# Performance work log

Hardware: AMD Instinct MI355X
Metric: run time of the kernel (lower is better)

Reference implementation:

```python
import jax, jax.numpy as jnp
import numpy as np
from jax import lax

B, C, H, W = 16, 256, 56, 56
GROUPS = 4
K = 3
DILATIONS = (1, 3, 5)
EPS = 1e-5


@jax.custom_vjp
def bin_act(x):
    return jnp.sign(x)

def _bin_act_fwd(x):
    return jnp.sign(x), x

def _bin_act_bwd(x, g):
    grad = jnp.where((x >= -1.0) & (x <= 0.0), 2.0 + 2.0 * x, 0.0) \
         + jnp.where((x > 0.0) & (x <= 1.0), 2.0 - 2.0 * x, 0.0)
    return (grad * g,)

bin_act.defvjp(_bin_act_fwd, _bin_act_bwd)


def _bin_weight(wi):
    # per-output-channel scaling from raw |w|, centered sign, clip-STE
    scale = lax.stop_gradient(jnp.mean(jnp.abs(wi), axis=(1, 2, 3), keepdims=True))
    wc = wi - jnp.mean(wi, axis=(1, 2, 3), keepdims=True)
    clipped = jnp.clip(wc, -1.0, 1.0)
    return lax.stop_gradient(scale * jnp.sign(wc) - clipped) + clipped


def setup_inputs() -> dict:
    key = jax.random.key(0)
    ks = jax.random.split(key, 3)
    x = jax.random.normal(ks[0], (B, C, H, W), dtype=jnp.float32)
    # 3 branches of grouped conv weights: (3, C_out, C_in/groups, K, K)
    w = jax.random.normal(ks[1], (3, C, C // GROUPS, K, K), dtype=jnp.float32) * 0.05
    cb = jax.random.normal(ks[2], (3, C), dtype=jnp.float32) * 0.01
    return {
        "x": x,
        "bias": jnp.zeros((1, C, 1, 1), jnp.float32),   # LearnableBias
        "w": w,
        "cb": cb,                                        # conv biases
        "move1": jnp.zeros((3, C), jnp.float32),
        "alpha": jnp.full((3, C), 0.25, jnp.float32),    # PReLU slopes
        "move2": jnp.zeros((3, C), jnp.float32),
        "gamma": jnp.ones((C,), jnp.float32),            # LayerNorm weight
        "beta": jnp.zeros((C,), jnp.float32),            # LayerNorm bias
    }


def reference(x, bias, w, cb, move1, alpha, move2, gamma, beta):
    xb = x + bias
    xq = bin_act(xb)  # binarized activations, shared across branches
    out = jnp.zeros_like(x)
    for i, d in enumerate(DILATIONS):
        wq = _bin_weight(w[i])
        y = lax.conv_general_dilated(
            xq, wq,
            window_strides=(1, 1),
            padding=[(d, d), (d, d)],  # 'same' for k=3 with dilation d
            rhs_dilation=(d, d),
            dimension_numbers=("NCHW", "OIHW", "NCHW"),
            feature_group_count=GROUPS,
        )
        y = y + cb[i][None, :, None, None]
        # RPReLU: shift, channel-wise PReLU, shift
        y = y - move1[i][None, :, None, None]
        y = jnp.where(y >= 0, y, alpha[i][None, :, None, None] * y)
        y = y + move2[i][None, :, None, None]
        out = out + y
    # LayerNorm over channel dim (equivalent to NHWC last-dim LN)
    mean = jnp.mean(out, axis=1, keepdims=True)
    var = jnp.var(out, axis=1, keepdims=True)
    out = (out - mean) * lax.rsqrt(var + EPS)
    out = out * gamma[None, :, None, None] + beta[None, :, None, None]
    return out
```

## Files before the change

### kernel.cpp

```cpp
#include <hip/hip_runtime.h>
#include <hip/hip_fp16.h>
#include <stdint.h>

static constexpr int Bc = 16, Cc = 256, Hc = 56, Wc = 56, Gc = 4, CGc = 64;
static constexpr int HWc = Hc * Wc;
static constexpr float EPSc = 1e-5f;
static constexpr int ROWP = 72;
static constexpr int COL0 = 8;


static constexpr int SBS = 260;

__global__ __launch_bounds__(256) void k_prep(
    const float* __restrict__ w, const float* __restrict__ x,
    const float* __restrict__ bias, uint64_t* __restrict__ wbits,
    float* __restrict__ scales, uint64_t* __restrict__ abits,
    uint32_t* __restrict__ zero_area) {
  const int t = threadIdx.x;
  if (blockIdx.x < 192) {
    const int io = blockIdx.x * 4 + (t >> 6);
    const int i = io >> 8, o = io & 255;
    const int lane = t & 63;
    const float* wp = w + (size_t)io * 576 + lane * 9;
    float v[9];
    float ssum = 0.f, sabs = 0.f;
#pragma unroll
    for (int k = 0; k < 9; ++k) {
      v[k] = wp[k];
      ssum += v[k];
      sabs += fabsf(v[k]);
    }
#pragma unroll
    for (int off = 32; off > 0; off >>= 1) {
      ssum += __shfl_down(ssum, off);
      sabs += __shfl_down(sabs, off);
    }
    const float mean = __shfl(ssum, 0) * (1.f / 576.f);
    const float scale = __shfl(sabs, 0) * (1.f / 576.f);
#pragma unroll
    for (int k = 0; k < 9; ++k) {
      unsigned long long m = __ballot(v[k] > mean);
      if (lane == 0) wbits[(i * 9 + k) * Cc + o] = m;
    }
    if (lane == 0) scales[io] = scale;
  } else if (blockIdx.x == 192) {
    zero_area[t] = 0;
  } else {
    __shared__ uint8_t sb[Wc * SBS];
    const int bid = blockIdx.x - 193;
    const int b = bid / Hc, h = bid % Hc;
    const float* xb = x + ((size_t)b * Cc) * HWc + h * Wc;
#pragma unroll
    for (int k = 0; k < 14; ++k) {
      const int idx = k * 256 + t;
      const int c = idx / 14, q = idx - c * 14;
      const float4 v = *(const float4*)(xb + (size_t)c * HWc + q * 4);
      const float bc = bias[c];
      sb[(q * 4 + 0) * SBS + c] = (v.x + bc > 0.f);
      sb[(q * 4 + 1) * SBS + c] = (v.y + bc > 0.f);
      sb[(q * 4 + 2) * SBS + c] = (v.z + bc > 0.f);
      sb[(q * 4 + 3) * SBS + c] = (v.w + bc > 0.f);
    }
    __syncthreads();
    for (int idx = t; idx < Gc * ROWP; idx += 256) {
      const int g = idx / ROWP, k = idx - g * ROWP;
      uint64_t word = 0;
      if (k >= COL0 && k < COL0 + Wc) {
        const int ww = k - COL0;
        const uint32_t* p = (const uint32_t*)(sb + ww * SBS + g * 64);
        uint64_t acc = 0;
#pragma unroll
        for (int dw = 0; dw < 16; ++dw) {
          const uint32_t d = p[dw];
          const uint32_t nib = (d | (d >> 7) | (d >> 14) | (d >> 21)) & 0xF;
          acc |= (uint64_t)nib << (4 * dw);
        }
        word = acc;
      }
      abits[(((size_t)b * Gc + g) * Hc + h) * ROWP + k] = word;
    }
  }
}

template <int D>
struct Branch {
  uint64_t wgt[9];
  const uint64_t *r0, *r1, *r2;
  int BM, ZL, ZR;
  float sc, cbm1, al;

  __device__ __forceinline__ void init(const uint64_t* __restrict__ wb,
                                       const uint64_t* rowbase,
                                       const uint64_t* zrowp, int h,
                                       float sc_, float cbm1_, float al_) {
    sc = sc_; cbm1 = cbm1_; al = al_;
    int z[9];
#pragma unroll
    for (int k = 0; k < 9; ++k) {
      wgt[k] = wb[k * Cc];
      z[k] = 64 - 2 * (int)__builtin_popcountll(wgt[k]);
    }
    const bool v0 = (h - D >= 0), v2 = (h + D < Hc);
    r0 = v0 ? (rowbase + (size_t)(h - D) * ROWP) : zrowp;
    r1 = rowbase + (size_t)h * ROWP;
    r2 = v2 ? (rowbase + (size_t)(h + D) * ROWP) : zrowp;
    const int Zrow = (v0 ? 0 : (z[0] + z[1] + z[2])) +
                     (v2 ? 0 : (z[6] + z[7] + z[8]));
    BM = 576 - Zrow;
    ZL = (v0 ? z[0] : 0) + z[3] + (v2 ? z[6] : 0);
    ZR = (v0 ? z[2] : 0) + z[5] + (v2 ? z[8] : 0);
  }

  __device__ __forceinline__ void accum8(int w0, int acc[8]) const {
#pragma unroll
    for (int kh = 0; kh < 3; ++kh) {
      const uint64_t* rp = (kh == 0) ? r0 : (kh == 1 ? r1 : r2);
      uint64_t seg[8 + 2 * D];
#pragma unroll
      for (int j = 0; j < 8 + 2 * D; ++j) seg[j] = rp[w0 - D + j];
#pragma unroll
      for (int ww = 0; ww < 8; ++ww) {
#pragma unroll
        for (int kw = 0; kw < 3; ++kw)
          acc[ww] +=
              (int)__builtin_popcountll(wgt[kh * 3 + kw] ^ seg[ww + D * kw]);
      }
    }
  }

  __device__ __forceinline__ void epi8(int w0, const int acc[8],
                                       float outf[8]) const {
#pragma unroll
    for (int ww = 0; ww < 8; ++ww) {
      const int w = w0 + ww;
      const int B = BM - ((w < D) ? ZL : 0) - ((w >= Wc - D) ? ZR : 0);
      const float y0 = fmaf(sc, (float)(B - 2 * acc[ww]), cbm1);
      outf[ww] += fmaxf(y0, 0.f) + al * fminf(y0, 0.f);
    }
  }
};

static constexpr int TS2 = 58;

__global__ __launch_bounds__(256, 4) void k_conv_ln(
    const uint64_t* __restrict__ abits, const uint64_t* __restrict__ zrowp,
    const uint64_t* __restrict__ wbits, const float* __restrict__ scales,
    const float* __restrict__ cb, const float* __restrict__ mv1,
    const float* __restrict__ al, const float* __restrict__ mv2,
    const float* __restrict__ gamma, const float* __restrict__ beta,
    float* __restrict__ out) {
  __shared__ __half out_tile[Cc * TS2];
  __shared__ float redu[4][Wc], redq[4][Wc];
  __shared__ float mstat[Wc], rstat[Wc];

  const int bid = blockIdx.x;
  const int b = bid / Hc, h = bid % Hc;
  const int t = threadIdx.x;
  const int gu = __builtin_amdgcn_readfirstlane(t >> 6);

  const uint64_t* rowbase = abits + ((size_t)b * Gc + gu) * Hc * ROWP + COL0;

  Branch<1> b0; Branch<3> b1; Branch<5> b2;
  b0.init(wbits + 0 * 9 * Cc + t, rowbase, zrowp, h, scales[0 * Cc + t],
          cb[0 * Cc + t] - mv1[0 * Cc + t], al[0 * Cc + t]);
  b1.init(wbits + 1 * 9 * Cc + t, rowbase, zrowp, h, scales[1 * Cc + t],
          cb[1 * Cc + t] - mv1[1 * Cc + t], al[1 * Cc + t]);
  b2.init(wbits + 2 * 9 * Cc + t, rowbase, zrowp, h, scales[2 * Cc + t],
          cb[2 * Cc + t] - mv1[2 * Cc + t], al[2 * Cc + t]);
  const float m2sum = mv2[0 * Cc + t] + mv2[1 * Cc + t] + mv2[2 * Cc + t];

  for (int ch = 0; ch < 7; ++ch) {
    const int w0 = ch * 8;
    float outf[8];
#pragma unroll
    for (int ww = 0; ww < 8; ++ww) outf[ww] = m2sum;
    { int acc[8] = {}; b0.accum8(w0, acc); b0.epi8(w0, acc, outf); }
    { int acc[8] = {}; b1.accum8(w0, acc); b1.epi8(w0, acc, outf); }
    { int acc[8] = {}; b2.accum8(w0, acc); b2.epi8(w0, acc, outf); }
#pragma unroll
    for (int ww = 0; ww < 8; ww += 2) {
      __half2 hv;
      hv.x = __float2half(outf[ww]);
      hv.y = __float2half(outf[ww + 1]);
      *(__half2*)&out_tile[t * TS2 + w0 + ww] = hv;
    }
  }
  __syncthreads();

  if (t < 4 * Wc) {
    const int ww = t % Wc;
    const int cq = t / Wc;
    float s = 0.f, sq = 0.f;
#pragma unroll 4
    for (int c = cq * 64; c < cq * 64 + 64; ++c) {
      const float v = __half2float(out_tile[c * TS2 + ww]);
      s += v;
      sq = fmaf(v, v, sq);
    }
    redu[cq][ww] = s;
    redq[cq][ww] = sq;
  }
  __syncthreads();
  if (t < Wc) {
    const float s = redu[0][t] + redu[1][t] + redu[2][t] + redu[3][t];
    const float sq = redq[0][t] + redq[1][t] + redq[2][t] + redq[3][t];
    const float mean = s * (1.f / 256.f);
    const float var = sq * (1.f / 256.f) - mean * mean;
    mstat[t] = mean;
    rstat[t] = rsqrtf(var + EPSc);
  }
  __syncthreads();

  float* base = out + ((size_t)b * Cc * Hc + h) * Wc;
  for (int idx = t; idx < Cc * Wc; idx += 256) {
    const int c = idx / Wc;
    const int ww = idx - c * Wc;
    const float v = __half2float(out_tile[c * TS2 + ww]);
    base[(size_t)c * HWc + ww] = (v - mstat[ww]) * rstat[ww] * gamma[c] + beta[c];
  }
}

extern "C" void kernel_launch(void* const* d_in, const int* in_sizes, int n_in,
                              void* d_out, int out_size, void* d_ws, size_t ws_size,
                              hipStream_t stream) {
  const float* x     = (const float*)d_in[0];
  const float* bias  = (const float*)d_in[1];
  const float* w     = (const float*)d_in[2];
  const float* cb    = (const float*)d_in[3];
  const float* mv1   = (const float*)d_in[4];
  const float* al    = (const float*)d_in[5];
  const float* mv2   = (const float*)d_in[6];
  const float* gamma = (const float*)d_in[7];
  const float* beta  = (const float*)d_in[8];
  float* out = (float*)d_out;

  uint8_t* ws = (uint8_t*)d_ws;
  uint32_t* zero_area = (uint32_t*)ws;
  const uint64_t* zrowp = (const uint64_t*)ws + COL0;
  uint64_t* abits = (uint64_t*)(ws + 1024);
  const size_t abits_bytes = (size_t)Bc * Gc * Hc * ROWP * 8;
  uint64_t* wbits = (uint64_t*)(ws + 1024 + abits_bytes);
  float* scales = (float*)(ws + 1024 + abits_bytes + 6912 * 8);

  hipLaunchKernelGGL(k_prep, dim3(192 + 1 + Bc * Hc), dim3(256), 0, stream,
                     w, x, bias, wbits, scales, abits, zero_area);
  hipLaunchKernelGGL(k_conv_ln, dim3(Bc * Hc), dim3(256), 0, stream,
                     abits, zrowp, wbits, scales, cb, mv1, al, mv2, gamma, beta,
                     out);
}
```

Measured before the change: 187.7 us.

## Pack activation bits with wave ballots and split conv rows into half-width blocks

The activation packing in the prep kernel now has each lane own one channel and uses wave ballots to build the 64-bit masks directly, replacing the shared-memory byte transpose. It also writes the zero padding columns itself. The conv+LayerNorm kernel now splits each output row into two 28-column halves, which doubles the grid to add parallelism and shrink the shared tile. The cost is that weight bits and per-branch setup are recomputed in both halves, and the chunk size drops to 7 columns with a non-unrolled loop.

Result: slower. 193.4 us (+3.1%).

```diff
diff --git a/kernel.cpp b/kernel.cpp
--- a/kernel.cpp
+++ b/kernel.cpp
@@ -2,14 +2,12 @@
 #include <hip/hip_fp16.h>
 #include <stdint.h>
 
-static constexpr int Bc = 16, Cc = 256, Hc = 56, Wc = 56, Gc = 4, CGc = 64;
+static constexpr int Bc = 16, Cc = 256, Hc = 56, Wc = 56, Gc = 4;
 static constexpr int HWc = Hc * Wc;
 static constexpr float EPSc = 1e-5f;
 static constexpr int ROWP = 72;
 static constexpr int COL0 = 8;
 
-
-static constexpr int SBS = 260;
 
 __global__ __launch_bounds__(256) void k_prep(
     const float* __restrict__ w, const float* __restrict__ x,
@@ -46,38 +44,30 @@
   } else if (blockIdx.x == 192) {
     zero_area[t] = 0;
   } else {
-    __shared__ uint8_t sb[Wc * SBS];
     const int bid = blockIdx.x - 193;
     const int b = bid / Hc, h = bid % Hc;
-    const float* xb = x + ((size_t)b * Cc) * HWc + h * Wc;
+    const int g = t >> 6, lane = t & 63;
+    const float* xp = x + ((size_t)(b * Cc + g * 64 + lane)) * HWc + h * Wc;
+    const float bc = bias[g * 64 + lane];
+    uint64_t* rowp = abits + (((size_t)b * Gc + g) * Hc + h) * ROWP;
+    if (lane < COL0) {
+      rowp[lane] = 0;
+      rowp[COL0 + Wc + lane] = 0;
+    }
 #pragma unroll
     for (int k = 0; k < 14; ++k) {
-      const int idx = k * 256 + t;
-      const int c = idx / 14, q = idx - c * 14;
-      const float4 v = *(const float4*)(xb + (size_t)c * HWc + q * 4);
-      const float bc = bias[c];
-      sb[(q * 4 + 0) * SBS + c] = (v.x + bc > 0.f);
-      sb[(q * 4 + 1) * SBS + c] = (v.y + bc > 0.f);
-      sb[(q * 4 + 2) * SBS + c] = (v.z + bc > 0.f);
-      sb[(q * 4 + 3) * SBS + c] = (v.w + bc > 0.f);
-    }
-    __syncthreads();
-    for (int idx = t; idx < Gc * ROWP; idx += 256) {
-      const int g = idx / ROWP, k = idx - g * ROWP;
-      uint64_t word = 0;
-      if (k >= COL0 && k < COL0 + Wc) {
-        const int ww = k - COL0;
-        const uint32_t* p = (const uint32_t*)(sb + ww * SBS + g * 64);
-        uint64_t acc = 0;
-#pragma unroll
-        for (int dw = 0; dw < 16; ++dw) {
-          const uint32_t d = p[dw];
-          const uint32_t nib = (d | (d >> 7) | (d >> 14) | (d >> 21)) & 0xF;
-          acc |= (uint64_t)nib << (4 * dw);
-        }
-        word = acc;
+      const float4 v = *(const float4*)(xp + k * 4);
+      const unsigned long long m0 = __ballot(v.x + bc > 0.f);
+      const unsigned long long m1 = __ballot(v.y + bc > 0.f);
+      const unsigned long long m2 = __ballot(v.z + bc > 0.f);
+      const unsigned long long m3 = __ballot(v.w + bc > 0.f);
+      if (lane == 0) {
+        ulonglong2 s01, s23;
+        s01.x = m0; s01.y = m1;
+        s23.x = m2; s23.y = m3;
+        *(ulonglong2*)(rowp + COL0 + 4 * k) = s01;
+        *(ulonglong2*)(rowp + COL0 + 4 * k + 2) = s23;
       }
-      abits[(((size_t)b * Gc + g) * Hc + h) * ROWP + k] = word;
     }
   }
 }
@@ -111,15 +101,16 @@
     ZR = (v0 ? z[2] : 0) + z[5] + (v2 ? z[8] : 0);
   }
 
-  __device__ __forceinline__ void accum8(int w0, int acc[8]) const {
+  template <int N>
+  __device__ __forceinline__ void accum(int w0, int acc[N]) const {
 #pragma unroll
     for (int kh = 0; kh < 3; ++kh) {
       const uint64_t* rp = (kh == 0) ? r0 : (kh == 1 ? r1 : r2);
-      uint64_t seg[8 + 2 * D];
-#pragma unroll
-      for (int j = 0; j < 8 + 2 * D; ++j) seg[j] = rp[w0 - D + j];
-#pragma unroll
-      for (int ww = 0; ww < 8; ++ww) {
+      uint64_t seg[N + 2 * D];
+#pragma unroll
+      for (int j = 0; j < N + 2 * D; ++j) seg[j] = rp[w0 - D + j];
+#pragma unroll
+      for (int ww = 0; ww < N; ++ww) {
 #pragma unroll
         for (int kw = 0; kw < 3; ++kw)
           acc[ww] +=
@@ -128,10 +119,11 @@
     }
   }
 
-  __device__ __forceinline__ void epi8(int w0, const int acc[8],
-                                       float outf[8]) const {
-#pragma unroll
-    for (int ww = 0; ww < 8; ++ww) {
+  template <int N>
+  __device__ __forceinline__ void epi(int w0, const int acc[N],
+                                      float outf[N]) const {
+#pragma unroll
+    for (int ww = 0; ww < N; ++ww) {
       const int w = w0 + ww;
       const int B = BM - ((w < D) ? ZL : 0) - ((w >= Wc - D) ? ZR : 0);
       const float y0 = fmaf(sc, (float)(B - 2 * acc[ww]), cbm1);
@@ -140,7 +132,9 @@
   }
 };
 
-static constexpr int TS2 = 58;
+static constexpr int WH = 28;
+static constexpr int TSH = 30;
+static constexpr int NCH = 7;
 
 __global__ __launch_bounds__(256, 4) void k_conv_ln(
     const uint64_t* __restrict__ abits, const uint64_t* __restrict__ zrowp,
@@ -149,12 +143,14 @@
     const float* __restrict__ al, const float* __restrict__ mv2,
     const float* __restrict__ gamma, const float* __restrict__ beta,
     float* __restrict__ out) {
-  __shared__ __half out_tile[Cc * TS2];
-  __shared__ float redu[4][Wc], redq[4][Wc];
-  __shared__ float mstat[Wc], rstat[Wc];
-
-  const int bid = blockIdx.x;
-  const int b = bid / Hc, h = bid % Hc;
+  __shared__ __half out_tile[Cc * TSH];
+  __shared__ float redu[4][WH], redq[4][WH];
+  __shared__ float mstat[WH], rstat[WH];
+
+  const int wh = blockIdx.x & 1;
+  const int bh = blockIdx.x >> 1;
+  const int b = bh / Hc, h = bh % Hc;
+  const int W0 = wh * WH;
   const int t = threadIdx.x;
   const int gu = __builtin_amdgcn_readfirstlane(t >> 6);
 
@@ -169,31 +165,28 @@
           cb[2 * Cc + t] - mv1[2 * Cc + t], al[2 * Cc + t]);
   const float m2sum = mv2[0 * Cc + t] + mv2[1 * Cc + t] + mv2[2 * Cc + t];
 
-  for (int ch = 0; ch < 7; ++ch) {
-    const int w0 = ch * 8;
-    float outf[8];
-#pragma unroll
-    for (int ww = 0; ww < 8; ++ww) outf[ww] = m2sum;
-    { int acc[8] = {}; b0.accum8(w0, acc); b0.epi8(w0, acc, outf); }
-    { int acc[8] = {}; b1.accum8(w0, acc); b1.epi8(w0, acc, outf); }
-    { int acc[8] = {}; b2.accum8(w0, acc); b2.epi8(w0, acc, outf); }
-#pragma unroll
-    for (int ww = 0; ww < 8; ww += 2) {
-      __half2 hv;
-      hv.x = __float2half(outf[ww]);
-      hv.y = __float2half(outf[ww + 1]);
-      *(__half2*)&out_tile[t * TS2 + w0 + ww] = hv;
-    }
+#pragma unroll 1
+  for (int ch = 0; ch < 4; ++ch) {
+    const int w0 = W0 + ch * NCH;
+    float outf[NCH];
+#pragma unroll
+    for (int ww = 0; ww < NCH; ++ww) outf[ww] = m2sum;
+    { int acc[NCH] = {}; b0.accum<NCH>(w0, acc); b0.epi<NCH>(w0, acc, outf); }
+    { int acc[NCH] = {}; b1.accum<NCH>(w0, acc); b1.epi<NCH>(w0, acc, outf); }
+    { int acc[NCH] = {}; b2.accum<NCH>(w0, acc); b2.epi<NCH>(w0, acc, outf); }
+#pragma unroll
+    for (int ww = 0; ww < NCH; ++ww)
+      out_tile[t * TSH + ch * NCH + ww] = __float2half(outf[ww]);
   }
   __syncthreads();
 
-  if (t < 4 * Wc) {
-    const int ww = t % Wc;
-    const int cq = t / Wc;
+  if (t < 4 * WH) {
+    const int ww = t % WH;
+    const int cq = t / WH;
     float s = 0.f, sq = 0.f;
 #pragma unroll 4
     for (int c = cq * 64; c < cq * 64 + 64; ++c) {
-      const float v = __half2float(out_tile[c * TS2 + ww]);
+      const float v = __half2float(out_tile[c * TSH + ww]);
       s += v;
       sq = fmaf(v, v, sq);
     }
@@ -201,7 +194,7 @@
     redq[cq][ww] = sq;
   }
   __syncthreads();
-  if (t < Wc) {
+  if (t < WH) {
     const float s = redu[0][t] + redu[1][t] + redu[2][t] + redu[3][t];
     const float sq = redq[0][t] + redq[1][t] + redq[2][t] + redq[3][t];
     const float mean = s * (1.f / 256.f);
@@ -211,11 +204,11 @@
   }
   __syncthreads();
 
-  float* base = out + ((size_t)b * Cc * Hc + h) * Wc;
-  for (int idx = t; idx < Cc * Wc; idx += 256) {
-    const int c = idx / Wc;
-    const int ww = idx - c * Wc;
-    const float v = __half2float(out_tile[c * TS2 + ww]);
+  float* base = out + ((size_t)b * Cc * Hc + h) * Wc + W0;
+  for (int idx = t; idx < Cc * WH; idx += 256) {
+    const int c = idx / WH;
+    const int ww = idx - c * WH;
+    const float v = __half2float(out_tile[c * TSH + ww]);
     base[(size_t)c * HWc + ww] = (v - mstat[ww]) * rstat[ww] * gamma[c] + beta[c];
   }
 }
@@ -244,7 +237,7 @@
 
   hipLaunchKernelGGL(k_prep, dim3(192 + 1 + Bc * Hc), dim3(256), 0, stream,
                      w, x, bias, wbits, scales, abits, zero_area);
-  hipLaunchKernelGGL(k_conv_ln, dim3(Bc * Hc), dim3(256), 0, stream,
+  hipLaunchKernelGGL(k_conv_ln, dim3(Bc * Hc * 2), dim3(256), 0, stream,
                      abits, zrowp, wbits, scales, cb, mv1, al, mv2, gamma, beta,
                      out);
 }
```

## Replace bit-packed popcount conv with int8 ±1 MFMA matrix products

Applied to the files above, without the earlier changes.

Weights and activations are stored as ±1 int8 bytes instead of packed 64-bit sign words. The grouped dilated conv becomes a sum of 32x32x32 int8 MFMA instructions per tap. The result is the dot product directly, so the zero-padding correction terms go away, and the prep kernel is split into half-channel blocks. This moves the work from VALU popcount onto the matrix cores, at the cost of 8x larger activation storage and more global traffic per row.

Result: slower. 417.3 us (+122.3%).

```diff
diff --git a/kernel.cpp b/kernel.cpp
--- a/kernel.cpp
+++ b/kernel.cpp
@@ -2,19 +2,24 @@
 #include <hip/hip_fp16.h>
 #include <stdint.h>
 
-static constexpr int Bc = 16, Cc = 256, Hc = 56, Wc = 56, Gc = 4, CGc = 64;
+static constexpr int Bc = 16, Cc = 256, Hc = 56, Wc = 56, Gc = 4;
 static constexpr int HWc = Hc * Wc;
 static constexpr float EPSc = 1e-5f;
-static constexpr int ROWP = 72;
+static constexpr int ROWB = 72;
 static constexpr int COL0 = 8;
-
-
-static constexpr int SBS = 260;
+static constexpr int ROWBYTES = ROWB * 64;
+static constexpr int ZBYTES = 8192;
+
+typedef int i32x4 __attribute__((ext_vector_type(4)));
+typedef int i32x16 __attribute__((ext_vector_type(16)));
+
+
+static constexpr int SBS2 = 132;
 
 __global__ __launch_bounds__(256) void k_prep(
     const float* __restrict__ w, const float* __restrict__ x,
-    const float* __restrict__ bias, uint64_t* __restrict__ wbits,
-    float* __restrict__ scales, uint64_t* __restrict__ abits,
+    const float* __restrict__ bias, uint8_t* __restrict__ wbytes,
+    float* __restrict__ scales, uint8_t* __restrict__ abytes,
     uint32_t* __restrict__ zero_area) {
   const int t = threadIdx.x;
   if (blockIdx.x < 192) {
@@ -37,119 +42,91 @@
     }
     const float mean = __shfl(ssum, 0) * (1.f / 576.f);
     const float scale = __shfl(sabs, 0) * (1.f / 576.f);
-#pragma unroll
-    for (int k = 0; k < 9; ++k) {
-      unsigned long long m = __ballot(v[k] > mean);
-      if (lane == 0) wbits[(i * 9 + k) * Cc + o] = m;
-    }
+    const int g = o >> 6, ol = o & 63;
+    uint8_t* dst = wbytes + ((size_t)(i * 4 + g) * 9) * 4096 + ol * 64 + lane;
+#pragma unroll
+    for (int k = 0; k < 9; ++k)
+      dst[k * 4096] = (v[k] > mean) ? (uint8_t)1 : (uint8_t)0xFF;
     if (lane == 0) scales[io] = scale;
   } else if (blockIdx.x == 192) {
-    zero_area[t] = 0;
+    uint4 z;
+    z.x = z.y = z.z = z.w = 0u;
+    ((uint4*)zero_area)[t] = z;
+    ((uint4*)zero_area)[t + 256] = z;
   } else {
-    __shared__ uint8_t sb[Wc * SBS];
+    __shared__ uint8_t sb[Wc * SBS2];
     const int bid = blockIdx.x - 193;
-    const int b = bid / Hc, h = bid % Hc;
-    const float* xb = x + ((size_t)b * Cc) * HWc + h * Wc;
-#pragma unroll
-    for (int k = 0; k < 14; ++k) {
+    const int b = bid / 112;
+    const int rem = bid - b * 112;
+    const int h = rem >> 1, chh = rem & 1;
+    const float* xb = x + ((size_t)(b * Cc + chh * 128)) * HWc + h * Wc;
+#pragma unroll
+    for (int k = 0; k < 7; ++k) {
       const int idx = k * 256 + t;
-      const int c = idx / 14, q = idx - c * 14;
-      const float4 v = *(const float4*)(xb + (size_t)c * HWc + q * 4);
-      const float bc = bias[c];
-      sb[(q * 4 + 0) * SBS + c] = (v.x + bc > 0.f);
-      sb[(q * 4 + 1) * SBS + c] = (v.y + bc > 0.f);
-      sb[(q * 4 + 2) * SBS + c] = (v.z + bc > 0.f);
-      sb[(q * 4 + 3) * SBS + c] = (v.w + bc > 0.f);
+      const int cl = idx / 14, q = idx - cl * 14;
+      const float4 v = *(const float4*)(xb + (size_t)cl * HWc + q * 4);
+      const float bc = bias[chh * 128 + cl];
+      sb[(q * 4 + 0) * SBS2 + cl] = (v.x + bc > 0.f) ? 1 : 0xFF;
+      sb[(q * 4 + 1) * SBS2 + cl] = (v.y + bc > 0.f) ? 1 : 0xFF;
+      sb[(q * 4 + 2) * SBS2 + cl] = (v.z + bc > 0.f) ? 1 : 0xFF;
+      sb[(q * 4 + 3) * SBS2 + cl] = (v.w + bc > 0.f) ? 1 : 0xFF;
     }
     __syncthreads();
-    for (int idx = t; idx < Gc * ROWP; idx += 256) {
-      const int g = idx / ROWP, k = idx - g * ROWP;
-      uint64_t word = 0;
-      if (k >= COL0 && k < COL0 + Wc) {
-        const int ww = k - COL0;
-        const uint32_t* p = (const uint32_t*)(sb + ww * SBS + g * 64);
-        uint64_t acc = 0;
-#pragma unroll
-        for (int dw = 0; dw < 16; ++dw) {
-          const uint32_t d = p[dw];
-          const uint32_t nib = (d | (d >> 7) | (d >> 14) | (d >> 21)) & 0xF;
-          acc |= (uint64_t)nib << (4 * dw);
-        }
-        word = acc;
-      }
-      abits[(((size_t)b * Gc + g) * Hc + h) * ROWP + k] = word;
+    for (int idx = t; idx < 2 * ROWB * 16; idx += 256) {
+      const int gl = idx / (ROWB * 16);
+      const int r = idx - gl * (ROWB * 16);
+      const int wp_ = r >> 4, d4 = r & 15;
+      uint32_t word = 0;
+      if (wp_ >= COL0 && wp_ < COL0 + Wc)
+        word = *(const uint32_t*)(sb + (wp_ - COL0) * SBS2 + gl * 64 + d4 * 4);
+      const int g = chh * 2 + gl;
+      *(uint32_t*)(abytes + ((size_t)((b * Gc + g) * Hc + h)) * ROWBYTES +
+                   wp_ * 64 + d4 * 4) = word;
     }
   }
 }
 
 template <int D>
-struct Branch {
-  uint64_t wgt[9];
-  const uint64_t *r0, *r1, *r2;
-  int BM, ZL, ZR;
-  float sc, cbm1, al;
-
-  __device__ __forceinline__ void init(const uint64_t* __restrict__ wb,
-                                       const uint64_t* rowbase,
-                                       const uint64_t* zrowp, int h,
-                                       float sc_, float cbm1_, float al_) {
-    sc = sc_; cbm1 = cbm1_; al = al_;
-    int z[9];
-#pragma unroll
-    for (int k = 0; k < 9; ++k) {
-      wgt[k] = wb[k * Cc];
-      z[k] = 64 - 2 * (int)__builtin_popcountll(wgt[k]);
-    }
-    const bool v0 = (h - D >= 0), v2 = (h + D < Hc);
-    r0 = v0 ? (rowbase + (size_t)(h - D) * ROWP) : zrowp;
-    r1 = rowbase + (size_t)h * ROWP;
-    r2 = v2 ? (rowbase + (size_t)(h + D) * ROWP) : zrowp;
-    const int Zrow = (v0 ? 0 : (z[0] + z[1] + z[2])) +
-                     (v2 ? 0 : (z[6] + z[7] + z[8]));
-    BM = 576 - Zrow;
-    ZL = (v0 ? z[0] : 0) + z[3] + (v2 ? z[6] : 0);
-    ZR = (v0 ? z[2] : 0) + z[5] + (v2 ? z[8] : 0);
-  }
-
-  __device__ __forceinline__ void accum8(int w0, int acc[8]) const {
-#pragma unroll
-    for (int kh = 0; kh < 3; ++kh) {
-      const uint64_t* rp = (kh == 0) ? r0 : (kh == 1 ? r1 : r2);
-      uint64_t seg[8 + 2 * D];
-#pragma unroll
-      for (int j = 0; j < 8 + 2 * D; ++j) seg[j] = rp[w0 - D + j];
-#pragma unroll
-      for (int ww = 0; ww < 8; ++ww) {
-#pragma unroll
-        for (int kw = 0; kw < 3; ++kw)
-          acc[ww] +=
-              (int)__builtin_popcountll(wgt[kh * 3 + kw] ^ seg[ww + D * kw]);
-      }
-    }
-  }
-
-  __device__ __forceinline__ void epi8(int w0, const int acc[8],
-                                       float outf[8]) const {
-#pragma unroll
-    for (int ww = 0; ww < 8; ++ww) {
-      const int w = w0 + ww;
-      const int B = BM - ((w < D) ? ZL : 0) - ((w >= Wc - D) ? ZR : 0);
-      const float y0 = fmaf(sc, (float)(B - 2 * acc[ww]), cbm1);
-      outf[ww] += fmaxf(y0, 0.f) + al * fminf(y0, 0.f);
-    }
-  }
-};
-
-static constexpr int TS2 = 58;
+__device__ __forceinline__ void branch_accum(
+    const uint8_t* __restrict__ r0, const uint8_t* __restrict__ r1,
+    const uint8_t* __restrict__ r2, const uint8_t* __restrict__ wb,
+    int ot2048, int laneoff, float sc, float cbm1, float alp,
+    float outf0[16], float outf1[16]) {
+  i32x16 ac0 = {0, 0, 0, 0, 0, 0, 0, 0, 0, 0, 0, 0, 0, 0, 0, 0};
+  i32x16 ac1 = {0, 0, 0, 0, 0, 0, 0, 0, 0, 0, 0, 0, 0, 0, 0, 0};
+#pragma unroll
+  for (int tap = 0; tap < 9; ++tap) {
+    const uint8_t* r = (tap < 3) ? r0 : ((tap < 6) ? r1 : r2);
+    const int wsh = (COL0 + D * ((tap % 3) - 1)) * 64 + laneoff;
+#pragma unroll
+    for (int ks = 0; ks < 2; ++ks) {
+      const i32x4 Bf =
+          *(const i32x4*)(wb + tap * 4096 + ot2048 + ks * 32 + laneoff);
+      const i32x4 A0 = *(const i32x4*)(r + wsh + ks * 32);
+      const i32x4 A1 = *(const i32x4*)(r + wsh + 2048 + ks * 32);
+      ac0 = __builtin_amdgcn_mfma_i32_32x32x32_i8(A0, Bf, ac0, 0, 0, 0);
+      ac1 = __builtin_amdgcn_mfma_i32_32x32x32_i8(A1, Bf, ac1, 0, 0, 0);
+    }
+  }
+#pragma unroll
+  for (int q = 0; q < 16; ++q) {
+    const float y0 = fmaf(sc, (float)ac0[q], cbm1);
+    outf0[q] += fmaxf(y0, 0.f) + alp * fminf(y0, 0.f);
+    const float y1 = fmaf(sc, (float)ac1[q], cbm1);
+    outf1[q] += fmaxf(y1, 0.f) + alp * fminf(y1, 0.f);
+  }
+}
+
+static constexpr int TS = 60;
 
 __global__ __launch_bounds__(256, 4) void k_conv_ln(
-    const uint64_t* __restrict__ abits, const uint64_t* __restrict__ zrowp,
-    const uint64_t* __restrict__ wbits, const float* __restrict__ scales,
+    const uint8_t* __restrict__ abytes, const uint8_t* __restrict__ zb,
+    const uint8_t* __restrict__ wbytes, const float* __restrict__ scales,
     const float* __restrict__ cb, const float* __restrict__ mv1,
     const float* __restrict__ al, const float* __restrict__ mv2,
     const float* __restrict__ gamma, const float* __restrict__ beta,
     float* __restrict__ out) {
-  __shared__ __half out_tile[Cc * TS2];
+  __shared__ __half out_tile[Cc * TS];
   __shared__ float redu[4][Wc], redq[4][Wc];
   __shared__ float mstat[Wc], rstat[Wc];
 
@@ -157,32 +134,47 @@
   const int b = bid / Hc, h = bid % Hc;
   const int t = threadIdx.x;
   const int gu = __builtin_amdgcn_readfirstlane(t >> 6);
-
-  const uint64_t* rowbase = abits + ((size_t)b * Gc + gu) * Hc * ROWP + COL0;
-
-  Branch<1> b0; Branch<3> b1; Branch<5> b2;
-  b0.init(wbits + 0 * 9 * Cc + t, rowbase, zrowp, h, scales[0 * Cc + t],
-          cb[0 * Cc + t] - mv1[0 * Cc + t], al[0 * Cc + t]);
-  b1.init(wbits + 1 * 9 * Cc + t, rowbase, zrowp, h, scales[1 * Cc + t],
-          cb[1 * Cc + t] - mv1[1 * Cc + t], al[1 * Cc + t]);
-  b2.init(wbits + 2 * 9 * Cc + t, rowbase, zrowp, h, scales[2 * Cc + t],
-          cb[2 * Cc + t] - mv1[2 * Cc + t], al[2 * Cc + t]);
-  const float m2sum = mv2[0 * Cc + t] + mv2[1 * Cc + t] + mv2[2 * Cc + t];
-
-  for (int ch = 0; ch < 7; ++ch) {
-    const int w0 = ch * 8;
-    float outf[8];
-#pragma unroll
-    for (int ww = 0; ww < 8; ++ww) outf[ww] = m2sum;
-    { int acc[8] = {}; b0.accum8(w0, acc); b0.epi8(w0, acc, outf); }
-    { int acc[8] = {}; b1.accum8(w0, acc); b1.epi8(w0, acc, outf); }
-    { int acc[8] = {}; b2.accum8(w0, acc); b2.epi8(w0, acc, outf); }
-#pragma unroll
-    for (int ww = 0; ww < 8; ww += 2) {
-      __half2 hv;
-      hv.x = __float2half(outf[ww]);
-      hv.y = __float2half(outf[ww + 1]);
-      *(__half2*)&out_tile[t * TS2 + w0 + ww] = hv;
+  const int lane = t & 63, lane31 = lane & 31;
+  const int laneoff = lane31 * 64 + (lane >> 5) * 16;
+
+  const uint8_t* ab_g = abytes + (size_t)((b * Gc + gu) * Hc) * ROWBYTES;
+  const uint8_t* r1m = (h - 1 >= 0) ? ab_g + (size_t)(h - 1) * ROWBYTES : zb;
+  const uint8_t* rmd = ab_g + (size_t)h * ROWBYTES;
+  const uint8_t* r1p = (h + 1 < Hc) ? ab_g + (size_t)(h + 1) * ROWBYTES : zb;
+  const uint8_t* r3m = (h - 3 >= 0) ? ab_g + (size_t)(h - 3) * ROWBYTES : zb;
+  const uint8_t* r3p = (h + 3 < Hc) ? ab_g + (size_t)(h + 3) * ROWBYTES : zb;
+  const uint8_t* r5m = (h - 5 >= 0) ? ab_g + (size_t)(h - 5) * ROWBYTES : zb;
+  const uint8_t* r5p = (h + 5 < Hc) ? ab_g + (size_t)(h + 5) * ROWBYTES : zb;
+
+  const uint8_t* wb0 = wbytes + (size_t)(0 * Gc + gu) * 9 * 4096;
+  const uint8_t* wb1 = wbytes + (size_t)(1 * Gc + gu) * 9 * 4096;
+  const uint8_t* wb2 = wbytes + (size_t)(2 * Gc + gu) * 9 * 4096;
+
+#pragma unroll 1
+  for (int ot = 0; ot < 2; ++ot) {
+    const int o = gu * 64 + ot * 32 + lane31;
+    const float sc0 = scales[o], sc1 = scales[256 + o], sc2 = scales[512 + o];
+    const float c0 = cb[o] - mv1[o];
+    const float c1 = cb[256 + o] - mv1[256 + o];
+    const float c2 = cb[512 + o] - mv1[512 + o];
+    const float a0 = al[o], a1 = al[256 + o], a2 = al[512 + o];
+    const float m2s = mv2[o] + mv2[256 + o] + mv2[512 + o];
+    float outf0[16], outf1[16];
+#pragma unroll
+    for (int q = 0; q < 16; ++q) {
+      outf0[q] = m2s;
+      outf1[q] = m2s;
+    }
+    const int ot2048 = ot * 2048;
+    branch_accum<1>(r1m, rmd, r1p, wb0, ot2048, laneoff, sc0, c0, a0, outf0, outf1);
+    branch_accum<3>(r3m, rmd, r3p, wb1, ot2048, laneoff, sc1, c1, a1, outf0, outf1);
+    branch_accum<5>(r5m, rmd, r5p, wb2, ot2048, laneoff, sc2, c2, a2, outf0, outf1);
+    const int wbse = 4 * (lane >> 5);
+#pragma unroll
+    for (int q = 0; q < 16; ++q) {
+      const int wl = (q & 3) + 8 * (q >> 2) + wbse;
+      out_tile[o * TS + wl] = __float2half(outf0[q]);
+      if (wl + 32 < Wc) out_tile[o * TS + 32 + wl] = __float2half(outf1[q]);
     }
   }
   __syncthreads();
@@ -193,7 +185,7 @@
     float s = 0.f, sq = 0.f;
 #pragma unroll 4
     for (int c = cq * 64; c < cq * 64 + 64; ++c) {
-      const float v = __half2float(out_tile[c * TS2 + ww]);
+      const float v = __half2float(out_tile[c * TS + ww]);
       s += v;
       sq = fmaf(v, v, sq);
     }
@@ -215,7 +207,7 @@
   for (int idx = t; idx < Cc * Wc; idx += 256) {
     const int c = idx / Wc;
     const int ww = idx - c * Wc;
-    const float v = __half2float(out_tile[c * TS2 + ww]);
+    const float v = __half2float(out_tile[c * TS + ww]);
     base[(size_t)c * HWc + ww] = (v - mstat[ww]) * rstat[ww] * gamma[c] + beta[c];
   }
 }
@@ -236,15 +228,15 @@
 
   uint8_t* ws = (uint8_t*)d_ws;
   uint32_t* zero_area = (uint32_t*)ws;
-  const uint64_t* zrowp = (const uint64_t*)ws + COL0;
-  uint64_t* abits = (uint64_t*)(ws + 1024);
-  const size_t abits_bytes = (size_t)Bc * Gc * Hc * ROWP * 8;
-  uint64_t* wbits = (uint64_t*)(ws + 1024 + abits_bytes);
-  float* scales = (float*)(ws + 1024 + abits_bytes + 6912 * 8);
-
-  hipLaunchKernelGGL(k_prep, dim3(192 + 1 + Bc * Hc), dim3(256), 0, stream,
-                     w, x, bias, wbits, scales, abits, zero_area);
+  const uint8_t* zb = ws;
+  uint8_t* abytes = ws + ZBYTES;
+  const size_t abytes_sz = (size_t)Bc * Gc * Hc * ROWBYTES;
+  uint8_t* wbytes = abytes + abytes_sz;
+  float* scales = (float*)(wbytes + (size_t)3 * Gc * 9 * 4096);
+
+  hipLaunchKernelGGL(k_prep, dim3(192 + 1 + Bc * Hc * 2), dim3(256), 0, stream,
+                     w, x, bias, wbytes, scales, abytes, zero_area);
   hipLaunchKernelGGL(k_conv_ln, dim3(Bc * Hc), dim3(256), 0, stream,
-                     abits, zrowp, wbits, scales, cb, mv1, al, mv2, gamma, beta,
+                     abytes, zb, wbytes, scales, cb, mv1, al, mv2, gamma, beta,
                      out);
 }
```
